# Kernel tuning notes

Measured on AMD Instinct MI355X. Metric: run time of the kernel, lower is better.

The kernel has to match this reference:

```python
import jax, jax.numpy as jnp
import numpy as np

EMBED_DIM = 768
NUM_HEADS = 12
HEAD_DIM = EMBED_DIM // NUM_HEADS
SCALE = HEAD_DIM ** -0.5


def setup_inputs() -> dict:
    key = jax.random.key(0)
    k_x, k_qkv, k_pw, k_pb = jax.random.split(key, 4)
    B, N = 2, 4096
    x = jax.random.normal(k_x, (B, N, EMBED_DIM), dtype=jnp.float32)
    # nn.Linear weights stored as [out, in]; we keep [in, out] for x @ W
    w_qkv = jax.random.normal(k_qkv, (EMBED_DIM, 3 * EMBED_DIM), dtype=jnp.float32) * (EMBED_DIM ** -0.5)
    w_proj = jax.random.normal(k_pw, (EMBED_DIM, EMBED_DIM), dtype=jnp.float32) * (EMBED_DIM ** -0.5)
    b_proj = jax.random.normal(k_pb, (EMBED_DIM,), dtype=jnp.float32) * 0.02
    return {"x": x, "w_qkv": w_qkv, "w_proj": w_proj, "b_proj": b_proj}


def reference(x, w_qkv, w_proj, b_proj):
    B, N, D = x.shape
    H, hd = NUM_HEADS, HEAD_DIM
    qkv = x @ w_qkv                                   # [B, N, 3*D]
    qkv = qkv.reshape(B, N, 3, H, hd)                 # matches '(qkv h d)' split order
    q, k, v = (qkv[:, :, i].transpose(0, 2, 1, 3) for i in range(3))  # each [B, H, N, hd]
    attn = jnp.einsum('bhid,bhjd->bhij', q, k) * SCALE  # [B, H, N, N] fully materialized
    attn = jax.nn.softmax(attn, axis=-1)
    out = jnp.einsum('bhij,bhjd->bhid', attn, v)        # [B, H, N, hd]
    out = out.transpose(0, 2, 1, 3).reshape(B, N, D)    # 'b h n d -> b n (h d)'
    return out @ w_proj + b_proj
```

## Files before the change

### kernel.cpp

```cpp
#include <hip/hip_runtime.h>
#include <hip/hip_bf16.h>

typedef __attribute__((ext_vector_type(4))) float f32x4;
typedef __attribute__((ext_vector_type(4))) int i32x4;
typedef __attribute__((ext_vector_type(8))) short s16x8;

static constexpr int NB = 2, NH = 12, SEQ = 4096, DM = 768, HD = 64;
static constexpr int ROWS = NB * SEQ;
static constexpr float QSC = 0.125f * 1.44269504f;

#define MFMA(a, b, c) __builtin_amdgcn_mfma_f32_16x16x32_bf16((a), (b), (c), 0, 0, 0)

typedef const void __attribute__((address_space(1)))* gas_t;
typedef void __attribute__((address_space(3)))* las_t;

__device__ __forceinline__ short f2bf(float f) {
  union { float f; unsigned u; } v; v.f = f;
  unsigned r = v.u + 0x7fffu + ((v.u >> 16) & 1u);
  return (short)(r >> 16);
}

__device__ __forceinline__ float exp2v(float x) {
  float r; asm("v_exp_f32 %0, %1" : "=v"(r) : "v"(x)); return r;
}

static constexpr int NC4 = ROWS * DM / 4 / 256;
static constexpr int NT1 = (DM / 32) * (3 * DM / 32);
static constexpr int NT2 = (DM / 32) * (DM / 32);

__device__ __forceinline__ void tcast_body(const float* __restrict__ in,
                                           short* __restrict__ out, int r, int c,
                                           int bid, short tile[32][33]) {
  int tpc = c >> 5;
  int by = bid / tpc, bx = bid % tpc;
  int tx = threadIdx.x & 31, ty = threadIdx.x >> 5;
#pragma unroll
  for (int i = 0; i < 4; ++i)
    tile[ty + i * 8][tx] = f2bf(in[(size_t)(by * 32 + ty + i * 8) * c + bx * 32 + tx]);
  __syncthreads();
#pragma unroll
  for (int i = 0; i < 4; ++i)
    out[(size_t)(bx * 32 + ty + i * 8) * r + by * 32 + tx] = tile[tx][ty + i * 8];
}

__global__ __launch_bounds__(256) void k_prep(const float* __restrict__ x,
                                              short* __restrict__ xb,
                                              const float* __restrict__ wqkv,
                                              short* __restrict__ wtqkv,
                                              const float* __restrict__ wproj,
                                              short* __restrict__ wtproj) {
  __shared__ short tile[32][33];
  int bid = blockIdx.x;
  if (bid < NC4) {
    int i = bid * 256 + threadIdx.x;
    float4 v = reinterpret_cast<const float4*>(x)[i];
    short4 o = { f2bf(v.x), f2bf(v.y), f2bf(v.z), f2bf(v.w) };
    reinterpret_cast<short4*>(xb)[i] = o;
  } else if (bid < NC4 + NT1) {
    tcast_body(wqkv, wtqkv, DM, 3 * DM, bid - NC4, tile);
  } else {
    tcast_body(wproj, wtproj, DM, DM, bid - NC4 - NT1, tile);
  }
}

__device__ __forceinline__ void gemm128(const short* __restrict__ A,
                                        const short* __restrict__ Bt,
                                        int K, int row0, int col0,
                                        short As[2][4096], short Bs[2][4096],
                                        f32x4 acc[4][4]) {
  int w = threadIdx.x >> 6, l = threadIdx.x & 63;
  int q = l & 15, g = l >> 4;
  int wr = w >> 1, wc = w & 1;
  int sr = w * 16 + (l >> 2);
  int sc = (l & 3) * 8;

#define STG(buf, k0)                                                           \
  {                                                                            \
    _Pragma("unroll")                                                          \
    for (int i = 0; i < 2; ++i) {                                              \
      __builtin_amdgcn_global_load_lds(                                        \
          (gas_t)(A + (size_t)(row0 + i * 64 + sr) * K + (k0) + sc),           \
          (las_t)&As[buf][i * 2048 + w * 512], 16, 0, 0);                      \
      __builtin_amdgcn_global_load_lds(                                        \
          (gas_t)(Bt + (size_t)(col0 + i * 64 + sr) * K + (k0) + sc),          \
          (las_t)&Bs[buf][i * 2048 + w * 512], 16, 0, 0);                      \
    }                                                                          \
  }

  STG(0, 0);
  __syncthreads();
  int cur = 0;
  for (int k0 = 0; k0 < K; k0 += 32) {
    if (k0 + 32 < K) STG(cur ^ 1, k0 + 32);
    s16x8 af[4], bf[4];
#pragma unroll
    for (int m = 0; m < 4; ++m)
      af[m] = *reinterpret_cast<const s16x8*>(&As[cur][(wr * 64 + m * 16 + q) * 32 + g * 8]);
#pragma unroll
    for (int n = 0; n < 4; ++n)
      bf[n] = *reinterpret_cast<const s16x8*>(&Bs[cur][(wc * 64 + n * 16 + q) * 32 + g * 8]);
#pragma unroll
    for (int m = 0; m < 4; ++m)
#pragma unroll
      for (int n = 0; n < 4; ++n)
        acc[m][n] = MFMA(bf[n], af[m], acc[m][n]);
    __syncthreads();
    cur ^= 1;
  }
#undef STG
}

__global__ __launch_bounds__(256) void k_gemm_qkv2(const short* __restrict__ xb,
                                                   const short* __restrict__ wt,
                                                   short* __restrict__ qw,
                                                   short* __restrict__ kw,
                                                   short* __restrict__ vtw) {
  __shared__ __align__(16) short As[2][4096], Bs[2][4096];
  int bid = blockIdx.x;
  int swz = (bid & 7) * 144 + (bid >> 3);
  int brow = swz / 18, bcol = swz % 18;
  int row0 = brow * 128, col0 = bcol * 128;
  f32x4 acc[4][4] = {};
  gemm128(xb, wt, DM, row0, col0, As, Bs, acc);

  int w = threadIdx.x >> 6, l = threadIdx.x & 63;
  int q = l & 15, g = l >> 4;
  int wr = w >> 1, wc = w & 1;
  int cb = col0 + wc * 64;
  int which = cb / DM, h = (cb % DM) >> 6;
  int rowb = row0 + wr * 64;
  int b = rowb >> 12;
  int bh = b * NH + h;
#pragma unroll
  for (int m = 0; m < 4; ++m) {
    int nseq = (rowb & 4095) + m * 16 + q;
#pragma unroll
    for (int n = 0; n < 4; ++n) {
      int d = n * 16 + g * 4;
      if (which == 2) {
#pragma unroll
        for (int r = 0; r < 4; ++r)
          vtw[((size_t)bh * HD + d + r) * SEQ + nseq] = f2bf(acc[m][n][r]);
      } else {
        short* dst = (which == 0) ? qw : kw;
        float sc = (which == 0) ? QSC : 1.f;
        short4 ov = { f2bf(acc[m][n][0] * sc), f2bf(acc[m][n][1] * sc),
                      f2bf(acc[m][n][2] * sc), f2bf(acc[m][n][3] * sc) };
        *reinterpret_cast<short4*>(&dst[((size_t)bh * SEQ + nseq) * HD + d]) = ov;
      }
    }
  }
}

__global__ __launch_bounds__(256) void k_gemm_proj2(const short* __restrict__ aob,
                                                    const short* __restrict__ wt,
                                                    const float* __restrict__ bias,
                                                    float* __restrict__ out) {
  __shared__ __align__(16) short As[2][4096], Bs[2][4096];
  int bid = blockIdx.x;
  int swz = (bid & 7) * 48 + (bid >> 3);
  int brow = swz / 6, bcol = swz % 6;
  int row0 = brow * 128, col0 = bcol * 128;
  f32x4 acc[4][4] = {};
  gemm128(aob, wt, DM, row0, col0, As, Bs, acc);

  int w = threadIdx.x >> 6, l = threadIdx.x & 63;
  int q = l & 15, g = l >> 4;
  int wr = w >> 1, wc = w & 1;
#pragma unroll
  for (int m = 0; m < 4; ++m) {
    int row = row0 + wr * 64 + m * 16 + q;
#pragma unroll
    for (int n = 0; n < 4; ++n) {
      int col = col0 + wc * 64 + n * 16 + g * 4;
      f32x4 bv = *reinterpret_cast<const f32x4*>(&bias[col]);
      f32x4 ov = acc[m][n] + bv;
      *reinterpret_cast<f32x4*>(&out[(size_t)row * DM + col]) = ov;
    }
  }
}

__global__ __launch_bounds__(256, 4) void k_attn12(const short* __restrict__ qw,
                                                   const short* __restrict__ kw,
                                                   const short* __restrict__ vtw,
                                                   short* __restrict__ ao) {
  __shared__ __align__(16) short lds[2][2][4096];

  int bid = blockIdx.x;
  int swz = (bid & 7) * 96 + (bid >> 3);
  int bh = swz >> 5;
  int qchunk = swz & 31;

  int w = threadIdx.x >> 6, l = threadIdx.x & 63;
  int q = l & 15, g = l >> 4;

  const short* Kg = kw + (size_t)bh * SEQ * HD;
  const short* Vg = vtw + (size_t)bh * HD * SEQ;

  int ss = (l & 7) ^ (l >> 3) ^ ((w & 1) << 2);
  int rst = w * 8 + (l >> 3);

  int qbase = qchunk * 128 + w * 32;
  s16x8 qf[2][2];
#pragma unroll
  for (int qt2 = 0; qt2 < 2; ++qt2)
#pragma unroll
    for (int kh = 0; kh < 2; ++kh)
      qf[qt2][kh] = *reinterpret_cast<const s16x8*>(
          qw + ((size_t)bh * SEQ + qbase + qt2 * 16 + q) * HD + kh * 32 + g * 8);

  s16x8 ones;
  {
    short o1 = (q == 0) ? (short)0x3F80 : (short)0;
#pragma unroll
    for (int i = 0; i < 8; ++i) ones[i] = o1;
  }

  f32x4 o[2][4] = {};
  f32x4 lsa[2] = {};

#define STAGE(buf, t)                                                              \
  {                                                                                \
    int key0 = (t) * 64;                                                           \
    _Pragma("unroll")                                                              \
    for (int i = 0; i < 2; ++i) {                                                  \
      const short* gk = Kg + (size_t)(key0 + i * 32 + rst) * HD + ss * 8;          \
      __builtin_amdgcn_global_load_lds((gas_t)gk,                                  \
          (las_t)&lds[buf][0][i * 2048 + w * 512], 16, 0, 0);                      \
      const short* gv = Vg + (size_t)(i * 32 + rst) * SEQ + key0 + ss * 8;         \
      __builtin_amdgcn_global_load_lds((gas_t)gv,                                  \
          (las_t)&lds[buf][1][i * 2048 + w * 512], 16, 0, 0);                      \
    }                                                                              \
  }

#define TBODY(CUR, NXT, tt, DO_STAGE)                                              \
  {                                                                                \
    if (DO_STAGE) STAGE(NXT, (tt) + 1);                                            \
    f32x4 s[2][2][2] = {};                             \
    __builtin_amdgcn_s_setprio(1);                                                 \
    _Pragma("unroll")                                                              \
    for (int c = 0; c < 2; ++c)                                                    \
      _Pragma("unroll")                                                            \
      for (int ab = 0; ab < 2; ++ab) {                                             \
        int R = c * 32 + ab * 4 + ((q >> 2) << 3) + (q & 3);                       \
        int sw = (R & 7) ^ (((R >> 3) & 1) << 2);                                  \
        _Pragma("unroll")                                                          \
        for (int kh = 0; kh < 2; ++kh) {                                           \
          int slot = (kh * 4 + g) ^ sw;                                            \
          s16x8 af = *reinterpret_cast<const s16x8*>(                              \
              &lds[CUR][0][R * 64 + slot * 8]);                                    \
          s[c][ab][0] = MFMA(af, qf[0][kh], s[c][ab][0]);                          \
          s[c][ab][1] = MFMA(af, qf[1][kh], s[c][ab][1]);                          \
        }                                                                          \
      }                                                                            \
    __builtin_amdgcn_s_setprio(0);                                                 \
    i32x4 pv[2][2];                                   \
    _Pragma("unroll")                                                              \
    for (int qt2 = 0; qt2 < 2; ++qt2) {                                            \
      unsigned u[16];                                                              \
      _Pragma("unroll")                                                            \
      for (int i = 0; i < 16; ++i)                                                 \
        u[i] = __float_as_uint(exp2v(s[i >> 3][(i >> 2) & 1][qt2][i & 3]));        \
      _Pragma("unroll")                                                            \
      for (int c = 0; c < 2; ++c)                                                  \
        _Pragma("unroll")                                                          \
        for (int j = 0; j < 4; ++j)                                                \
          pv[c][qt2][j] = (int)__builtin_amdgcn_perm(u[c * 8 + 2 * j + 1],         \
                                                     u[c * 8 + 2 * j],             \
                                                     0x07060302u);                 \
    }                                                                              \
    __builtin_amdgcn_s_setprio(1);                                                 \
    _Pragma("unroll")                                                              \
    for (int c = 0; c < 2; ++c) {                                                  \
      s16x8 p0 = __builtin_bit_cast(s16x8, pv[c][0]);                              \
      s16x8 p1 = __builtin_bit_cast(s16x8, pv[c][1]);                              \
      _Pragma("unroll")                                                            \
      for (int dt = 0; dt < 4; ++dt) {                                             \
        int R = dt * 16 + q;                                                       \
        int sw = (R & 7) ^ (((R >> 3) & 1) << 2);                                  \
        int slot = (c * 4 + g) ^ sw;                                               \
        s16x8 vf = *reinterpret_cast<const s16x8*>(                                \
            &lds[CUR][1][R * 64 + slot * 8]);                                      \
        o[0][dt] = MFMA(vf, p0, o[0][dt]);                                         \
        o[1][dt] = MFMA(vf, p1, o[1][dt]);                                         \
      }                                                                            \
      lsa[0] = MFMA(ones, p0, lsa[0]);                                             \
      lsa[1] = MFMA(ones, p1, lsa[1]);                                             \
    }                                                                              \
    __builtin_amdgcn_s_setprio(0);                                                 \
    __syncthreads();                                                               \
  }

  STAGE(0, 0);
  __syncthreads();

  for (int t = 0; t < SEQ / 64 - 2; t += 2) {
    TBODY(0, 1, t, true);
    TBODY(1, 0, t + 1, true);
  }
  TBODY(0, 1, SEQ / 64 - 2, true);
  TBODY(1, 0, SEQ / 64 - 1, false);
#undef TBODY
#undef STAGE

  int b = bh / NH, h = bh % NH;
  float ls0 = __shfl(lsa[0][0], q);
  float ls1 = __shfl(lsa[1][0], q);
  float inv[2] = { 1.f / ls0, 1.f / ls1 };
#pragma unroll
  for (int qt2 = 0; qt2 < 2; ++qt2) {
    size_t row = (size_t)b * SEQ + qbase + qt2 * 16 + q;
    short* op = ao + row * DM + h * HD;
#pragma unroll
    for (int dt = 0; dt < 4; ++dt) {
      short4 ov = { f2bf(o[qt2][dt][0] * inv[qt2]), f2bf(o[qt2][dt][1] * inv[qt2]),
                    f2bf(o[qt2][dt][2] * inv[qt2]), f2bf(o[qt2][dt][3] * inv[qt2]) };
      *reinterpret_cast<short4*>(op + dt * 16 + g * 4) = ov;
    }
  }
}

extern "C" void kernel_launch(void* const* d_in, const int* in_sizes, int n_in,
                              void* d_out, int out_size, void* d_ws, size_t ws_size,
                              hipStream_t stream) {
  const float* x      = (const float*)d_in[0];
  const float* w_qkv  = (const float*)d_in[1];
  const float* w_proj = (const float*)d_in[2];
  const float* b_proj = (const float*)d_in[3];
  float* out = (float*)d_out;

  char* p = (char*)d_ws;
  auto take = [&](size_t bytes) { char* r = p; p += (bytes + 255) & ~(size_t)255; return r; };
  short* xb     = (short*)take((size_t)ROWS * DM * 2);
  short* wtqkv  = (short*)take((size_t)3 * DM * DM * 2);
  short* wtproj = (short*)take((size_t)DM * DM * 2);
  short* qw     = (short*)take((size_t)NB * NH * SEQ * HD * 2);
  short* kw     = (short*)take((size_t)NB * NH * SEQ * HD * 2);
  short* vtw    = (short*)take((size_t)NB * NH * HD * SEQ * 2);
  short* ao     = (short*)take((size_t)ROWS * DM * 2);

  k_prep<<<NC4 + NT1 + NT2, 256, 0, stream>>>(x, xb, w_qkv, wtqkv, w_proj, wtproj);
  k_gemm_qkv2<<<64 * 18, 256, 0, stream>>>(xb, wtqkv, qw, kw, vtw);
  k_attn12<<<NB * NH * (SEQ / 128), 256, 0, stream>>>(qw, kw, vtw, ao);
  k_gemm_proj2<<<64 * 6, 256, 0, stream>>>(ao, wtproj, b_proj, out);
}
```

Before: 177.0 us.

## Triple-buffer attention K/V tiles and prefetch next K fragments into registers

The attention kernel moves from double to triple LDS buffering, staging K/V tiles two iterations ahead. It also loads the next tile's K fragments into registers during the softmax/PV phase, so the QK^T MFMAs do not wait on LDS reads. The cost is more LDS per block and more registers, with launch bounds dropped from 4 to 3 blocks per CU. Lower occupancy may hurt latency hiding elsewhere.

```diff
diff --git a/kernel.cpp b/kernel.cpp
--- a/kernel.cpp
+++ b/kernel.cpp
@@ -180,11 +180,11 @@
   }
 }
 
-__global__ __launch_bounds__(256, 4) void k_attn12(const short* __restrict__ qw,
+__global__ __launch_bounds__(256, 3) void k_attn15(const short* __restrict__ qw,
                                                    const short* __restrict__ kw,
                                                    const short* __restrict__ vtw,
                                                    short* __restrict__ ao) {
-  __shared__ __align__(16) short lds[2][2][4096];
+  __shared__ __align__(16) short lds[3][2][4096];
 
   int bid = blockIdx.x;
   int swz = (bid & 7) * 96 + (bid >> 3);
@@ -218,6 +218,7 @@
 
   f32x4 o[2][4] = {};
   f32x4 lsa[2] = {};
+  s16x8 kf[8];
 
 #define STAGE(buf, t)                                                              \
   {                                                                                \
@@ -233,11 +234,8 @@
     }                                                                              \
   }
 
-#define TBODY(CUR, NXT, tt, DO_STAGE)                                              \
+#define LDK(BUF)                                                                   \
   {                                                                                \
-    if (DO_STAGE) STAGE(NXT, (tt) + 1);                                            \
-    f32x4 s[2][2][2] = {};                             \
-    __builtin_amdgcn_s_setprio(1);                                                 \
     _Pragma("unroll")                                                              \
     for (int c = 0; c < 2; ++c)                                                    \
       _Pragma("unroll")                                                            \
@@ -247,13 +245,29 @@
         _Pragma("unroll")                                                          \
         for (int kh = 0; kh < 2; ++kh) {                                           \
           int slot = (kh * 4 + g) ^ sw;                                            \
-          s16x8 af = *reinterpret_cast<const s16x8*>(                              \
-              &lds[CUR][0][R * 64 + slot * 8]);                                    \
+          kf[c * 4 + ab * 2 + kh] = *reinterpret_cast<const s16x8*>(               \
+              &lds[BUF][0][R * 64 + slot * 8]);                                    \
+        }                                                                          \
+      }                                                                            \
+  }
+
+#define TBODY(BCUR, BN, BC, tt)                                                    \
+  {                                                                                \
+    if ((tt) + 2 < SEQ / 64) STAGE(BC, (tt) + 2);                                  \
+    f32x4 s[2][2][2] = {};                             \
+    __builtin_amdgcn_s_setprio(1);                                                 \
+    _Pragma("unroll")                                                              \
+    for (int c = 0; c < 2; ++c)                                                    \
+      _Pragma("unroll")                                                            \
+      for (int ab = 0; ab < 2; ++ab)                                               \
+        _Pragma("unroll")                                                          \
+        for (int kh = 0; kh < 2; ++kh) {                                           \
+          s16x8 af = kf[c * 4 + ab * 2 + kh];                                      \
           s[c][ab][0] = MFMA(af, qf[0][kh], s[c][ab][0]);                          \
           s[c][ab][1] = MFMA(af, qf[1][kh], s[c][ab][1]);                          \
         }                                                                          \
-      }                                                                            \
     __builtin_amdgcn_s_setprio(0);                                                 \
+    if ((tt) + 1 < SEQ / 64) LDK(BN);                                              \
     i32x4 pv[2][2];                                   \
     _Pragma("unroll")                                                              \
     for (int qt2 = 0; qt2 < 2; ++qt2) {                                            \
@@ -280,7 +294,7 @@
         int sw = (R & 7) ^ (((R >> 3) & 1) << 2);                                  \
         int slot = (c * 4 + g) ^ sw;                                               \
         s16x8 vf = *reinterpret_cast<const s16x8*>(                                \
-            &lds[CUR][1][R * 64 + slot * 8]);                                      \
+            &lds[BCUR][1][R * 64 + slot * 8]);                                     \
         o[0][dt] = MFMA(vf, p0, o[0][dt]);                                         \
         o[1][dt] = MFMA(vf, p1, o[1][dt]);                                         \
       }                                                                            \
@@ -292,15 +306,18 @@
   }
 
   STAGE(0, 0);
+  STAGE(1, 1);
   __syncthreads();
-
-  for (int t = 0; t < SEQ / 64 - 2; t += 2) {
-    TBODY(0, 1, t, true);
-    TBODY(1, 0, t + 1, true);
-  }
-  TBODY(0, 1, SEQ / 64 - 2, true);
-  TBODY(1, 0, SEQ / 64 - 1, false);
+  LDK(0);
+
+  for (int t = 0; t < SEQ / 64 - 1; t += 3) {
+    TBODY(0, 1, 2, t);
+    TBODY(1, 2, 0, t + 1);
+    TBODY(2, 0, 1, t + 2);
+  }
+  TBODY(0, 1, 2, SEQ / 64 - 1);
 #undef TBODY
+#undef LDK
 #undef STAGE
 
   int b = bh / NH, h = bh % NH;
@@ -341,6 +358,6 @@
 
   k_prep<<<NC4 + NT1 + NT2, 256, 0, stream>>>(x, xb, w_qkv, wtqkv, w_proj, wtproj);
   k_gemm_qkv2<<<64 * 18, 256, 0, stream>>>(xb, wtqkv, qw, kw, vtw);
-  k_attn12<<<NB * NH * (SEQ / 128), 256, 0, stream>>>(qw, kw, vtw, ao);
+  k_attn15<<<NB * NH * (SEQ / 128), 256, 0, stream>>>(qw, kw, vtw, ao);
   k_gemm_proj2<<<64 * 6, 256, 0, stream>>>(ao, wtproj, b_proj, out);
 }
```

New measurement: 175.8 us. About the same (-0.7%).
